# Kernel tuning notes

Measured on AMD Instinct MI355X. Metric: run time of the kernel, lower is better.

Reference implementation:

```python
import jax, jax.numpy as jnp
import numpy as np

D_EMB = 1024
N_HEADS = 16
HEAD_DIM = D_EMB // N_HEADS


def _xavier(key, out_f, in_f):
    limit = jnp.sqrt(6.0 / (in_f + out_f))
    return jax.random.uniform(key, (out_f, in_f), jnp.float32, -limit, limit)


def setup_inputs() -> dict:
    key = jax.random.key(0)
    k_x, k_qkv, k_out = jax.random.split(key, 3)
    x = jax.random.normal(k_x, (4, 2048, D_EMB), jnp.float32)
    # torch nn.Linear weights: [out_features, in_features], xavier_uniform; biases zero
    w_qkv = _xavier(k_qkv, 3 * D_EMB, D_EMB)
    b_qkv = jnp.zeros((3 * D_EMB,), jnp.float32)
    w_out = _xavier(k_out, D_EMB, D_EMB)
    b_out = jnp.zeros((D_EMB,), jnp.float32)
    return {"x": x, "w_qkv": w_qkv, "b_qkv": b_qkv, "w_out": w_out, "b_out": b_out}


def reference(x, w_qkv, b_qkv, w_out, b_out):
    B, S, D = x.shape
    # QKV projection: y = x @ W^T + b -> [B, S, 3D]
    qkv = jnp.einsum('bsd,ed->bse', x, w_qkv) + b_qkv
    # view(B, S, H, 3*head_dim) then split into q, k, v (matches torch chunk on last dim)
    qkv = qkv.reshape(B, S, N_HEADS, 3 * HEAD_DIM)
    q, k, v = jnp.split(qkv, 3, axis=-1)  # each [B, S, H, head_dim]
    scale = 1.0 / jnp.sqrt(jnp.float32(HEAD_DIM))
    scores = jnp.einsum('bshd,bthd->bhst', q, k) * scale  # [B, H, S, S]
    probs = jax.nn.softmax(scores, axis=-1)
    out = jnp.einsum('bhst,bthd->bshd', probs, v).reshape(B, S, D)
    return jnp.einsum('bsd,ed->bse', out, w_out) + b_out
```

## Files before the change

### kernel.cpp

```cpp
#include <hip/hip_runtime.h>

typedef __bf16 bf16_t;
typedef __bf16 bf16x8 __attribute__((ext_vector_type(8)));
typedef __bf16 bf16x4 __attribute__((ext_vector_type(4)));
typedef float f32x4 __attribute__((ext_vector_type(4)));

#define S_LEN 2048
#define D_EMB 1024
#define NH 16

#define MFMA16(a, b, c) __builtin_amdgcn_mfma_f32_16x16x32_bf16((a), (b), (c), 0, 0, 0)

__device__ __forceinline__ void gld16(void* lds, const void* g) {
  __builtin_amdgcn_global_load_lds(
      (__attribute__((address_space(1))) void*)(void*)(g),
      (__attribute__((address_space(3))) void*)(lds), 16, 0, 0);
}

__device__ __forceinline__ float exp2_hw(float x) {
  float r;
  asm("v_exp_f32 %0, %1" : "=v"(r) : "v"(x));
  return r;
}

__global__ __launch_bounds__(256) void cvt_bf16(const float* __restrict__ in,
                                                bf16_t* __restrict__ out, int n4) {
  int i = blockIdx.x * 256 + threadIdx.x;
  if (i >= n4) return;
  float4 v = ((const float4*)in)[i];
  bf16x4 o;
  o[0] = (bf16_t)v.x; o[1] = (bf16_t)v.y; o[2] = (bf16_t)v.z; o[3] = (bf16_t)v.w;
  ((bf16x4*)out)[i] = o;
}

template <int EPI>
__global__ __launch_bounds__(256) void gemm_bt(
    const bf16_t* __restrict__ A, const bf16_t* __restrict__ W,
    const float* __restrict__ bias, float* __restrict__ outF,
    bf16_t* __restrict__ outQ, int M, int N, int K) {
  __shared__ __attribute__((aligned(16))) bf16_t As[2][128 * 64];
  __shared__ __attribute__((aligned(16))) bf16_t Ws[2][128 * 64];
  const int tid = threadIdx.x;
  const int lane = tid & 63;
  const int wid = tid >> 6;
  const int l15 = lane & 15, lg = lane >> 4;
  int lin = blockIdx.x + gridDim.x * blockIdx.y;
  const int nwg = gridDim.x * gridDim.y;
  lin = (lin & 7) * (nwg >> 3) + (lin >> 3);
  const int tm = (lin / gridDim.x) * 128, tn = (lin % gridDim.x) * 128;
  const int wm = (wid >> 1) * 64, wn = (wid & 1) * 64;
  f32x4 acc[4][4] = {};
  const int q0 = tid * 16;

  auto stage = [&](int k0, int buf) {
#pragma unroll
    for (int i = 0; i < 4; ++i) {
      int q = q0 + i * 4096;
      int row = q >> 7;
      int scb = (q & 127) ^ ((row & 7) << 4);
      gld16((char*)As[buf] + (q & ~1023),
            (const char*)A + ((size_t)(tm + row) * K + k0) * 2 + scb);
      gld16((char*)Ws[buf] + (q & ~1023),
            (const char*)W + ((size_t)(tn + row) * K + k0) * 2 + scb);
    }
  };

  stage(0, 0);
  __syncthreads();

  const int nkt = K >> 6;
  for (int it = 0; it < nkt; ++it) {
    const int cur = it & 1;
    if (it + 1 < nkt) stage((it + 1) << 6, cur ^ 1);
#pragma unroll
    for (int kk = 0; kk < 2; ++kk) {
      const int cb = kk * 64 + lg * 16;
      bf16x8 af[4], bfr[4];
#pragma unroll
      for (int mi = 0; mi < 4; ++mi) {
        int row = wm + mi * 16 + l15;
        af[mi] = *(const bf16x8*)((const char*)As[cur] + row * 128 +
                                  (cb ^ ((row & 7) << 4)));
      }
#pragma unroll
      for (int ni = 0; ni < 4; ++ni) {
        int row = wn + ni * 16 + l15;
        bfr[ni] = *(const bf16x8*)((const char*)Ws[cur] + row * 128 +
                                   (cb ^ ((row & 7) << 4)));
      }
#pragma unroll
      for (int mi = 0; mi < 4; ++mi)
#pragma unroll
        for (int ni = 0; ni < 4; ++ni)
          acc[mi][ni] = MFMA16(af[mi], bfr[ni], acc[mi][ni]);
    }
    if (it + 1 < nkt) __syncthreads();
  }

  if (EPI == 0) {
#pragma unroll
    for (int mi = 0; mi < 4; ++mi)
#pragma unroll
      for (int ni = 0; ni < 4; ++ni) {
        int colg = tn + wn + ni * 16 + l15;
        float bv = bias[colg];
#pragma unroll
        for (int j = 0; j < 4; ++j) {
          int rowg = tm + wm + mi * 16 + lg * 4 + j;
          outF[(size_t)rowg * N + colg] = acc[mi][ni][j] + bv;
        }
      }
  } else {
#pragma unroll
    for (int mi = 0; mi < 4; ++mi)
#pragma unroll
      for (int ni = 0; ni < 4; ++ni) {
        int e = tn + wn + ni * 16 + l15;
        float bv = bias[e];
        int h = e / 192;
        int r = e - h * 192;
        int t = r >> 6, c = r & 63;
#pragma unroll
        for (int j = 0; j < 4; ++j) {
          int m = tm + wm + mi * 16 + lg * 4 + j;
          int b = m >> 11, s = m & 2047;
          float v = acc[mi][ni][j] + bv;
          if (t == 0) v *= 0.18033688011112042f;
          size_t base = ((size_t)(b * NH + h) * 3 + t) * (size_t)(S_LEN * 64);
          size_t idx;
          if (t == 2) {
            int rs = s & 31;
            int rp = (((rs >> 2) & 3) << 3) | ((rs >> 4) << 2) | (rs & 3);
            idx = base + (size_t)c * S_LEN + (size_t)((s & ~31) | rp);
          } else {
            idx = base + (size_t)s * 64 + c;
          }
          outQ[idx] = (bf16_t)v;
        }
      }
  }
}

__global__ __launch_bounds__(256, 2) void attn_fwd(const bf16_t* __restrict__ qkvb,
                                                   bf16_t* __restrict__ attnb) {
  __shared__ __attribute__((aligned(16))) bf16_t Ks[3][64 * 64];
  __shared__ __attribute__((aligned(16))) bf16_t Vs[3][64 * 64];
  const int tid = threadIdx.x, lane = tid & 63, wid = tid >> 6;
  const int l15 = lane & 15, lg = lane >> 4;
  int lin = blockIdx.x + (blockIdx.y << 3);
  lin = (lin & 7) * 64 + (lin >> 3);
  const int qt = lin & 7;
  const int bh = lin >> 3;
  const int b = bh >> 4, h = bh & 15;
  const char* Qg = (const char*)qkvb + (size_t)bh * 3 * (S_LEN * 64) * 2;
  const char* Kg = Qg + (size_t)S_LEN * 64 * 2;
  const char* Vtg = Kg + (size_t)S_LEN * 64 * 2;
  const int q0 = tid * 16;

  bf16x8 qf[4][2];
#pragma unroll
  for (int mi = 0; mi < 4; ++mi) {
    const char* qr = Qg + (size_t)(qt * 256 + wid * 64 + mi * 16 + l15) * 128;
#pragma unroll
    for (int kb = 0; kb < 2; ++kb)
      qf[mi][kb] = *(const bf16x8*)(qr + kb * 64 + lg * 16);
  }

  auto stageK = [&](int t) {
#pragma unroll
    for (int i = 0; i < 2; ++i) {
      int q = q0 + i * 4096;
      int row = q >> 7;
      int scb = (q & 127) ^ ((row & 7) << 4);
      gld16((char*)Ks[t % 3] + (q & ~1023), Kg + (size_t)(t * 64 + row) * 128 + scb);
    }
  };
  auto stageV = [&](int t) {
#pragma unroll
    for (int i = 0; i < 2; ++i) {
      int q = q0 + i * 4096;
      int row = q >> 7;
      int scb = (q & 127) ^ ((row & 7) << 4);
      gld16((char*)Vs[t % 3] + (q & ~1023),
            Vtg + (size_t)row * (S_LEN * 2) + t * 128 + scb);
    }
  };

  f32x4 o[4][4] = {};
  f32x4 den[4] = {};
  bf16x8 pf[2][4];
  bf16x8 onesf;
#pragma unroll
  for (int j = 0; j < 8; ++j) onesf[j] = (bf16_t)1.0f;
  const int swk = (l15 & 7) << 4;

  auto QK = [&](const bf16_t* Kc, f32x4(&stv)[4][4]) {
#pragma unroll
    for (int nk = 0; nk < 4; ++nk) {
      const char* kr = (const char*)Kc + (nk * 16 + l15) * 128;
      bf16x8 kf0 = *(const bf16x8*)(kr + ((lg * 16) ^ swk));
      bf16x8 kf1 = *(const bf16x8*)(kr + ((64 + lg * 16) ^ swk));
#pragma unroll
      for (int mi = 0; mi < 4; ++mi) {
        f32x4 z = {};
        z = MFMA16(kf0, qf[mi][0], z);
        stv[mi][nk] = MFMA16(kf1, qf[mi][1], z);
      }
    }
  };
  auto SM = [&](f32x4(&stv)[4][4]) {
#pragma unroll
    for (int mi = 0; mi < 4; ++mi)
#pragma unroll
      for (int nk = 0; nk < 4; ++nk)
#pragma unroll
        for (int j = 0; j < 4; ++j)
          stv[mi][nk][j] = exp2_hw(stv[mi][nk][j]);
#pragma unroll
    for (int kp = 0; kp < 2; ++kp)
#pragma unroll
      for (int mi = 0; mi < 4; ++mi)
#pragma unroll
        for (int j = 0; j < 4; ++j) {
          pf[kp][mi][j] = (bf16_t)stv[mi][2 * kp][j];
          pf[kp][mi][4 + j] = (bf16_t)stv[mi][2 * kp + 1][j];
        }
  };
  auto PV = [&](const bf16_t* Vc) {
#pragma unroll
    for (int kp = 0; kp < 2; ++kp) {
#pragma unroll
      for (int ndv = 0; ndv < 4; ++ndv) {
        const char* vr = (const char*)Vc + (ndv * 16 + l15) * 128;
        bf16x8 vf = *(const bf16x8*)(vr + ((kp * 64 + 16 * lg) ^ swk));
#pragma unroll
        for (int mi = 0; mi < 4; ++mi)
          o[mi][ndv] = MFMA16(pf[kp][mi], vf, o[mi][ndv]);
      }
#pragma unroll
      for (int mi = 0; mi < 4; ++mi)
        den[mi] = MFMA16(pf[kp][mi], onesf, den[mi]);
    }
  };

  stageV(0); stageK(0); stageV(1); stageK(1); stageK(2);
  asm volatile("s_waitcnt vmcnt(6)" ::: "memory");
  __builtin_amdgcn_s_barrier();
  asm volatile("" ::: "memory");
  {
    f32x4 stv[4][4];
    __builtin_amdgcn_s_setprio(1);
    QK(Ks[0], stv);
    __builtin_amdgcn_s_setprio(0);
    SM(stv);
  }

  for (int kt = 0; kt < 30; ++kt) {
    asm volatile("s_waitcnt vmcnt(2)" ::: "memory");
    __builtin_amdgcn_s_barrier();
    asm volatile("" ::: "memory");
    stageV(kt + 2);
    if (kt + 3 < 32) stageK(kt + 3);
    f32x4 stv[4][4];
    __builtin_amdgcn_s_setprio(1);
    QK(Ks[(kt + 1) % 3], stv);
    PV(Vs[kt % 3]);
    __builtin_amdgcn_s_setprio(0);
    SM(stv);
  }
  asm volatile("s_waitcnt vmcnt(0)" ::: "memory");
  __builtin_amdgcn_s_barrier();
  asm volatile("" ::: "memory");
  {
    f32x4 stv[4][4];
    __builtin_amdgcn_s_setprio(1);
    QK(Ks[31 % 3], stv);
    PV(Vs[30 % 3]);
    __builtin_amdgcn_s_setprio(0);
    SM(stv);
  }
  PV(Vs[31 % 3]);

  float inv[4][4];
#pragma unroll
  for (int mi = 0; mi < 4; ++mi)
#pragma unroll
    for (int j = 0; j < 4; ++j)
      inv[mi][j] = 1.0f / den[mi][j];

#pragma unroll
  for (int mi = 0; mi < 4; ++mi)
#pragma unroll
    for (int j = 0; j < 4; ++j) {
      int srow = qt * 256 + wid * 64 + mi * 16 + lg * 4 + j;
      bf16_t* dst = attnb + ((size_t)b * S_LEN + srow) * D_EMB + h * 64;
#pragma unroll
      for (int ndv = 0; ndv < 4; ++ndv)
        dst[ndv * 16 + l15] = (bf16_t)(o[mi][ndv][j] * inv[mi][j]);
    }
}

extern "C" void kernel_launch(void* const* d_in, const int* in_sizes, int n_in,
                              void* d_out, int out_size, void* d_ws, size_t ws_size,
                              hipStream_t stream) {
  const float* x = (const float*)d_in[0];
  const float* w_qkv = (const float*)d_in[1];
  const float* b_qkv = (const float*)d_in[2];
  const float* w_out = (const float*)d_in[3];
  const float* b_out = (const float*)d_in[4];
  float* out = (float*)d_out;

  bf16_t* xb = (bf16_t*)d_ws;
  bf16_t* wqkvb = xb + 8388608;
  bf16_t* woutb = wqkvb + 3145728;
  bf16_t* qkvb = woutb + 1048576;
  bf16_t* attnb = qkvb + 25165824;

  cvt_bf16<<<8192, 256, 0, stream>>>(x, xb, 2097152);
  cvt_bf16<<<3072, 256, 0, stream>>>(w_qkv, wqkvb, 786432);
  cvt_bf16<<<1024, 256, 0, stream>>>(w_out, woutb, 262144);

  gemm_bt<1><<<dim3(24, 64), 256, 0, stream>>>(xb, wqkvb, b_qkv, nullptr, qkvb,
                                               8192, 3072, 1024);
  attn_fwd<<<dim3(8, 64), 256, 0, stream>>>(qkvb, attnb);
  gemm_bt<0><<<dim3(8, 64), 256, 0, stream>>>(attnb, woutb, b_out, out, nullptr,
                                              8192, 1024, 1024);
}
```

Measured before the change: 175.5 us.

## Replace QKV GEMM with 256x256-tile, 8-wave ping-pong pipelined kernel

Adds a dedicated QKV projection kernel that uses 256x256 output tiles with 512 threads (8 waves). It splits each K step into quarter/half loads interleaved with MFMA phases under barriers and priority hints, keeping global-to-LDS loads overlapped with compute. The goal is more operand reuse per tile and better latency hiding than the old 128x128 generic GEMM. The trade-off is large LDS use (128KB), many barriers, and fewer blocks (384) on the grid. The epilogue is meant to reproduce the old layout: scaled Q and permuted V.

```diff
diff --git a/kernel.cpp b/kernel.cpp
--- a/kernel.cpp
+++ b/kernel.cpp
@@ -10,6 +10,10 @@
 #define NH 16
 
 #define MFMA16(a, b, c) __builtin_amdgcn_mfma_f32_16x16x32_bf16((a), (b), (c), 0, 0, 0)
+#define BARRIER()                        \
+  asm volatile("" ::: "memory");         \
+  __builtin_amdgcn_s_barrier();          \
+  asm volatile("" ::: "memory")
 
 __device__ __forceinline__ void gld16(void* lds, const void* g) {
   __builtin_amdgcn_global_load_lds(
@@ -31,6 +35,148 @@
   bf16x4 o;
   o[0] = (bf16_t)v.x; o[1] = (bf16_t)v.y; o[2] = (bf16_t)v.z; o[3] = (bf16_t)v.w;
   ((bf16x4*)out)[i] = o;
+}
+
+__global__ __launch_bounds__(512, 2) void gemm_qkv_8p(
+    const bf16_t* __restrict__ A, const bf16_t* __restrict__ W,
+    const float* __restrict__ bias, bf16_t* __restrict__ outQ) {
+  const int K = 1024;
+  __shared__ __attribute__((aligned(16))) bf16_t As[2][256 * 64];
+  __shared__ __attribute__((aligned(16))) bf16_t Ws[2][256 * 64];
+  const int tid = threadIdx.x, lane = tid & 63, wid = tid >> 6;
+  const int l15 = lane & 15, lg = lane >> 4;
+  const int wm = wid >> 2, wn = wid & 3;
+  int lin = blockIdx.x + 12 * blockIdx.y;
+  lin = (lin & 7) * 48 + (lin >> 3);
+  const int tm = (lin / 12) * 256, tn = (lin % 12) * 256;
+  const int q0 = tid * 16;
+
+  auto stAq = [&](int kt, int quad, int slot) {
+    int row = q0 >> 7;
+    int scb = (q0 & 127) ^ ((row & 7) << 4);
+    gld16((char*)As[slot] + quad * 8192 + (q0 & ~1023),
+          (const char*)A + ((size_t)(tm + quad * 64 + row) * K + kt * 64) * 2 + scb);
+  };
+  auto stWh = [&](int kt, int half, int slot) {
+#pragma unroll
+    for (int i = 0; i < 2; ++i) {
+      int q = q0 + i * 8192;
+      int row = q >> 7;
+      int scb = (q & 127) ^ ((row & 7) << 4);
+      gld16((char*)Ws[slot] + half * 16384 + (q & ~1023),
+            (const char*)W + ((size_t)(tn + half * 128 + row) * K + kt * 64) * 2 + scb);
+    }
+  };
+  auto rdA = [&](int slot, int mh, int kk, bf16x8(&af)[4]) {
+#pragma unroll
+    for (int m2 = 0; m2 < 4; ++m2) {
+      int row = wm * 128 + mh * 64 + m2 * 16 + l15;
+      af[m2] = *(const bf16x8*)((const char*)As[slot] + row * 128 +
+                                ((kk * 64 + lg * 16) ^ ((row & 7) << 4)));
+    }
+  };
+  auto rdB = [&](int slot, int kk, bf16x8(&bf)[4]) {
+#pragma unroll
+    for (int ni = 0; ni < 4; ++ni) {
+      int col = wn * 64 + ni * 16 + l15;
+      bf[ni] = *(const bf16x8*)((const char*)Ws[slot] + col * 128 +
+                                ((kk * 64 + lg * 16) ^ ((col & 7) << 4)));
+    }
+  };
+
+  f32x4 acc[8][4] = {};
+  bf16x8 af[4], bf0[4], bf1[4];
+  auto mm = [&](int mh, bf16x8(&a)[4], bf16x8(&b)[4]) {
+    __builtin_amdgcn_s_setprio(1);
+#pragma unroll
+    for (int m2 = 0; m2 < 4; ++m2)
+#pragma unroll
+      for (int ni = 0; ni < 4; ++ni)
+        acc[mh * 4 + m2][ni] = MFMA16(a[m2], b[ni], acc[mh * 4 + m2][ni]);
+    __builtin_amdgcn_s_setprio(0);
+  };
+
+  stWh(0, 0, 0); stWh(0, 1, 0);
+  stAq(0, 0, 0); stAq(0, 2, 0); stAq(0, 1, 0); stAq(0, 3, 0);
+  stWh(1, 0, 1); stWh(1, 1, 1);
+
+  for (int t = 0; t < 8; ++t) {
+    const int e = 2 * t, o = 2 * t + 1;
+    asm volatile("s_waitcnt vmcnt(4)" ::: "memory");
+    BARRIER();
+    stAq(o, 0, 1); stAq(o, 2, 1);
+    rdA(0, 0, 0, af); rdB(0, 0, bf0);
+    BARRIER();
+    mm(0, af, bf0);
+    BARRIER();
+    stAq(o, 1, 1); stAq(o, 3, 1);
+    rdA(0, 0, 1, af); rdB(0, 1, bf1);
+    BARRIER();
+    mm(0, af, bf1);
+    BARRIER();
+    if (t < 7) stWh(e + 2, 0, 0);
+    rdA(0, 1, 0, af);
+    BARRIER();
+    mm(1, af, bf0);
+    BARRIER();
+    if (t < 7) stWh(e + 2, 1, 0);
+    rdA(0, 1, 1, af);
+    BARRIER();
+    mm(1, af, bf1);
+    if (t < 7) {
+      asm volatile("s_waitcnt vmcnt(4)" ::: "memory");
+    } else {
+      asm volatile("s_waitcnt vmcnt(0)" ::: "memory");
+    }
+    BARRIER();
+    if (t < 7) { stAq(e + 2, 0, 0); stAq(e + 2, 2, 0); }
+    rdA(1, 0, 0, af); rdB(1, 0, bf0);
+    BARRIER();
+    mm(0, af, bf0);
+    BARRIER();
+    if (t < 7) { stAq(e + 2, 1, 0); stAq(e + 2, 3, 0); }
+    rdA(1, 0, 1, af); rdB(1, 1, bf1);
+    BARRIER();
+    mm(0, af, bf1);
+    BARRIER();
+    if (t < 7) stWh(o + 2, 0, 1);
+    rdA(1, 1, 0, af);
+    BARRIER();
+    mm(1, af, bf0);
+    BARRIER();
+    if (t < 7) stWh(o + 2, 1, 1);
+    rdA(1, 1, 1, af);
+    BARRIER();
+    mm(1, af, bf1);
+  }
+
+#pragma unroll
+  for (int mi = 0; mi < 8; ++mi)
+#pragma unroll
+    for (int ni = 0; ni < 4; ++ni) {
+      int e = tn + wn * 64 + ni * 16 + l15;
+      float bv = bias[e];
+      int h = e / 192;
+      int r = e - h * 192;
+      int tt = r >> 6, c = r & 63;
+#pragma unroll
+      for (int j = 0; j < 4; ++j) {
+        int m = tm + wm * 128 + mi * 16 + lg * 4 + j;
+        int b = m >> 11, s = m & 2047;
+        float v = acc[mi][ni][j] + bv;
+        if (tt == 0) v *= 0.18033688011112042f;
+        size_t base = ((size_t)(b * NH + h) * 3 + tt) * (size_t)(S_LEN * 64);
+        size_t idx;
+        if (tt == 2) {
+          int rs = s & 31;
+          int rp = (((rs >> 2) & 3) << 3) | ((rs >> 4) << 2) | (rs & 3);
+          idx = base + (size_t)c * S_LEN + (size_t)((s & ~31) | rp);
+        } else {
+          idx = base + (size_t)s * 64 + c;
+        }
+        outQ[idx] = (bf16_t)v;
+      }
+    }
 }
 
 template <int EPI>
@@ -320,8 +466,7 @@
   cvt_bf16<<<3072, 256, 0, stream>>>(w_qkv, wqkvb, 786432);
   cvt_bf16<<<1024, 256, 0, stream>>>(w_out, woutb, 262144);
 
-  gemm_bt<1><<<dim3(24, 64), 256, 0, stream>>>(xb, wqkvb, b_qkv, nullptr, qkvb,
-                                               8192, 3072, 1024);
+  gemm_qkv_8p<<<dim3(12, 32), 512, 0, stream>>>(xb, wqkvb, b_qkv, qkvb);
   attn_fwd<<<dim3(8, 64), 256, 0, stream>>>(qkvb, attnb);
   gemm_bt<0><<<dim3(8, 64), 256, 0, stream>>>(attnb, woutb, b_out, out, nullptr,
                                               8192, 1024, 1024);
```

After: 182.8 us. 4.2% more time.

## Add dedicated 256x192-tile QKV GEMM kernel with 512 threads and single-buffered LDS

Applied to the files above, without the earlier changes.

Replaces the generic 128x128 double-buffered QKV projection GEMM with a specialized kernel that uses 256x192 tiles, 8 waves per block and a single LDS buffer. The output tile width matches one head's q/k/v span, and the epilogue scatters directly into the head-major layout with the softmax scale folded into Q and a permuted V layout. Larger tiles raise arithmetic intensity and cut global reloads. In exchange, single buffering removes load/compute overlap within a block and relies on two blocks per CU to hide latency, and register pressure rises with 24 accumulators per wave.

```diff
diff --git a/kernel.cpp b/kernel.cpp
--- a/kernel.cpp
+++ b/kernel.cpp
@@ -31,6 +31,104 @@
   bf16x4 o;
   o[0] = (bf16_t)v.x; o[1] = (bf16_t)v.y; o[2] = (bf16_t)v.z; o[3] = (bf16_t)v.w;
   ((bf16x4*)out)[i] = o;
+}
+
+__global__ __launch_bounds__(512, 2) void gemm_qkv_sb(
+    const bf16_t* __restrict__ A, const bf16_t* __restrict__ W,
+    const float* __restrict__ bias, bf16_t* __restrict__ outQ) {
+  const int K = 1024;
+  __shared__ __attribute__((aligned(16))) bf16_t As[256 * 64];
+  __shared__ __attribute__((aligned(16))) bf16_t Ws[192 * 64];
+  const int tid = threadIdx.x, lane = tid & 63, wid = tid >> 6;
+  const int l15 = lane & 15, lg = lane >> 4;
+  const int wm = wid >> 2, wn = wid & 3;
+  int lin = blockIdx.x + 16 * blockIdx.y;
+  lin = (lin & 7) * 64 + (lin >> 3);
+  const int tm = (lin >> 4) * 256, tn = (lin & 15) * 192;
+  const int q0 = tid * 16;
+
+  auto stage = [&](int kt) {
+#pragma unroll
+    for (int i = 0; i < 4; ++i) {
+      int q = q0 + i * 8192;
+      int row = q >> 7;
+      int scb = (q & 127) ^ ((row & 7) << 4);
+      gld16((char*)As + (q & ~1023),
+            (const char*)A + ((size_t)(tm + row) * K + kt * 64) * 2 + scb);
+    }
+#pragma unroll
+    for (int i = 0; i < 3; ++i) {
+      int q = q0 + i * 8192;
+      int row = q >> 7;
+      int scb = (q & 127) ^ ((row & 7) << 4);
+      gld16((char*)Ws + (q & ~1023),
+            (const char*)W + ((size_t)(tn + row) * K + kt * 64) * 2 + scb);
+    }
+  };
+
+  f32x4 acc[8][3] = {};
+
+  for (int kt = 0; kt < 16; ++kt) {
+    stage(kt);
+    __syncthreads();
+#pragma unroll
+    for (int kk = 0; kk < 2; ++kk) {
+      const int cb = kk * 64 + lg * 16;
+      bf16x8 bfr[3];
+#pragma unroll
+      for (int ni = 0; ni < 3; ++ni) {
+        int col = wn * 48 + ni * 16 + l15;
+        bfr[ni] = *(const bf16x8*)((const char*)Ws + col * 128 +
+                                   (cb ^ ((col & 7) << 4)));
+      }
+#pragma unroll
+      for (int mh = 0; mh < 2; ++mh) {
+        bf16x8 af[4];
+#pragma unroll
+        for (int m2 = 0; m2 < 4; ++m2) {
+          int row = wm * 128 + mh * 64 + m2 * 16 + l15;
+          af[m2] = *(const bf16x8*)((const char*)As + row * 128 +
+                                    (cb ^ ((row & 7) << 4)));
+        }
+        __builtin_amdgcn_s_setprio(1);
+#pragma unroll
+        for (int m2 = 0; m2 < 4; ++m2)
+#pragma unroll
+          for (int ni = 0; ni < 3; ++ni)
+            acc[mh * 4 + m2][ni] = MFMA16(af[m2], bfr[ni], acc[mh * 4 + m2][ni]);
+        __builtin_amdgcn_s_setprio(0);
+      }
+    }
+    if (kt < 15) __syncthreads();
+  }
+
+#pragma unroll
+  for (int mi = 0; mi < 8; ++mi)
+#pragma unroll
+    for (int ni = 0; ni < 3; ++ni) {
+      int e = tn + wn * 48 + ni * 16 + l15;
+      float bv = bias[e];
+      int h = e / 192;
+      int r = e - h * 192;
+      int tt = r >> 6, c = r & 63;
+#pragma unroll
+      for (int j = 0; j < 4; ++j) {
+        int m = tm + wm * 128 + mi * 16 + lg * 4 + j;
+        int b = m >> 11, s = m & 2047;
+        float v = acc[mi][ni][j] + bv;
+        if (tt == 0) v *= 0.18033688011112042f;
+        size_t base = ((size_t)(b * NH + h) * 3 + tt) * (size_t)(S_LEN * 64);
+        size_t idx;
+        if (tt == 2) {
+          int rs = s & 31;
+          int rp = (((rs >> 2) & 3) << 3) | ((rs >> 4) << 2) | (rs & 3);
+          idx = base + (size_t)c * S_LEN + (size_t)((s & ~31) | rp);
+        } else {
+          idx = base + (size_t)s * 64 + c;
+        }
+        outQ[idx] = (bf16_t)v;
+      }
+    }
 }
 
 template <int EPI>
@@ -320,8 +418,7 @@
   cvt_bf16<<<3072, 256, 0, stream>>>(w_qkv, wqkvb, 786432);
   cvt_bf16<<<1024, 256, 0, stream>>>(w_out, woutb, 262144);
 
-  gemm_bt<1><<<dim3(24, 64), 256, 0, stream>>>(xb, wqkvb, b_qkv, nullptr, qkvb,
-                                               8192, 3072, 1024);
+  gemm_qkv_sb<<<dim3(16, 32), 512, 0, stream>>>(xb, wqkvb, b_qkv, qkvb);
   attn_fwd<<<dim3(8, 64), 256, 0, stream>>>(qkvb, attnb);
   gemm_bt<0><<<dim3(8, 64), 256, 0, stream>>>(attnb, woutb, b_out, out, nullptr,
                                               8192, 1024, 1024);
```

After: 174.9 us. About the same (-0.3%).
